# Performance work log

Hardware: AMD Instinct MI355X
Metric: run time of the kernel (lower is better)

Reference implementation:

```python
import jax, jax.numpy as jnp
import numpy as np

# --- module hyperparameters (match init_kwargs) ---
B, CIN, COUT, K = 32, 2, 2, 16
FEAT_DIM = 256
FRAME_SIZE, OVERLAP = 160, 40
NUM_FRAMES = 500
NUM_SAMPLES = NUM_FRAMES * FRAME_SIZE
FFT_SIZE = 512  # 2**ceil(log2(2*frame_size + overlap))
SHAPE_GAIN_DB = -6.0
GAIN_LIMITS_DB = (-6.0, 6.0)
LN10_DIV_20 = 0.11512925464970229


def setup_inputs() -> dict:
    key = jax.random.key(0)
    ks = jax.random.split(key, 6)
    x = jax.random.normal(ks[0], (B, CIN, NUM_SAMPLES), dtype=jnp.float32)
    features = jax.random.normal(ks[1], (B, NUM_FRAMES, FEAT_DIM), dtype=jnp.float32)
    # nn.Linear(feature_dim, in*out*K) and nn.Linear(feature_dim, out) params
    conv_kernel_w = jax.random.normal(ks[2], (COUT * CIN * K, FEAT_DIM), jnp.float32) / np.float32(np.sqrt(FEAT_DIM))
    conv_kernel_b = jax.random.normal(ks[3], (COUT * CIN * K,), jnp.float32) * 0.01
    filter_gain_w = jax.random.normal(ks[4], (COUT, FEAT_DIM), jnp.float32) / np.float32(np.sqrt(FEAT_DIM))
    filter_gain_b = jax.random.normal(ks[5], (COUT,), jnp.float32) * 0.01
    # fixed raised-cosine fade-out window (requires_grad=False buffer)
    n = jnp.arange(OVERLAP, dtype=jnp.float32)
    overlap_win = 0.5 + 0.5 * jnp.cos((n + 0.5) * jnp.pi / OVERLAP)
    return {"x": x, "features": features,
            "conv_kernel_w": conv_kernel_w, "conv_kernel_b": conv_kernel_b,
            "filter_gain_w": filter_gain_w, "filter_gain_b": filter_gain_b,
            "overlap_win": overlap_win}


def _forward(x, features, ck_w, ck_b, fg_w, fg_b, overlap_win):
    B_, F_, _ = features.shape
    log_min = GAIN_LIMITS_DB[0] * LN10_DIV_20
    log_max = GAIN_LIMITS_DB[1] * LN10_DIV_20
    gain_a = (log_max - log_min) / 2.0
    gain_b = (log_max + log_min) / 2.0
    shape_gain = min(1.0, 10.0 ** (SHAPE_GAIN_DB / 20.0))
    id_tap = K - 1 - K // 2  # padding[1]

    # per-frame kernels: (B, F, Cout, Cin, K)
    ck = (features @ ck_w.T + ck_b).reshape(B_, F_, COUT, CIN, K)
    # norm_p = 2 over (Cin, K)
    ck = ck / (1e-6 + jnp.sqrt(jnp.sum(ck * ck, axis=(-2, -1), keepdims=True)))
    idk = jnp.zeros_like(ck).at[..., id_tap].set(1.0)
    ck = shape_gain * ck + (1.0 - shape_gain) * idk
    gains = jnp.exp(gain_a * jnp.tanh(features @ fg_w.T + fg_b) + gain_b)  # (B,F,Cout)
    w = jnp.transpose(ck * gains[..., None, None], (0, 2, 3, 1, 4))  # (B,Cout,Cin,F,K)

    win1 = jnp.flip(overlap_win)  # fade-in (expansion_power == 1)
    win2 = overlap_win            # fade-out (== 1 - win1)

    # frame the input with K-1 lookback and OVERLAP lookahead samples
    xp = jnp.pad(x, ((0, 0), (0, 0), (K - 1, OVERLAP)))
    L = FRAME_SIZE + K - 1 + OVERLAP
    idx = jnp.arange(F_)[:, None] * FRAME_SIZE + jnp.arange(L)[None, :]
    frames = xp[:, :, idx]  # (B, Cin, F, L)

    # FFT convolution, summing over input channels in the frequency domain
    X = jnp.fft.rfft(frames, n=FFT_SIZE)          # (B,Cin,F,nf)
    Wf = jnp.fft.rfft(w, n=FFT_SIZE)              # (B,Cout,Cin,F,nf)
    Yf = jnp.einsum('bifn,boifn->bofn', X, Wf)
    Y = jnp.fft.irfft(Yf, n=FFT_SIZE)[..., K - 1: K - 1 + FRAME_SIZE + OVERLAP]  # (B,Cout,F,fs+ov)

    # windowed overlap-add crossfade between consecutive frame filters
    head = Y[..., :FRAME_SIZE].at[..., :OVERLAP].multiply(win1)
    tail = Y[..., FRAME_SIZE:] * win2  # (B,Cout,F,ov)
    out = head.at[:, :, 1:, :OVERLAP].add(tail[:, :, :-1])
    return out.reshape(B_, COUT, F_ * FRAME_SIZE)


def reference(x, features, conv_kernel_w, conv_kernel_b, filter_gain_w, filter_gain_b, overlap_win):
    return _forward(x, features, conv_kernel_w, conv_kernel_b, filter_gain_w, filter_gain_b, overlap_win)
```

## Files before the change

### kernel.cpp

```cpp
#include <hip/hip_runtime.h>

#define BB    32
#define NF    500
#define FRAME 160
#define OV    40
#define KK    16
#define NS    (NF * FRAME)
#define FEAT  256

#define NBODY (BB * 2 * NF * 15)
#define NOV   (BB * 2 * NF * 5)

__device__ const float GAIN_A     = 0.6907755278982137f;
__device__ const float SHAPE_GAIN = 0.5011872336272722f;

__global__ __launch_bounds__(1024) void wcalc3_kernel(
    const float* __restrict__ feats,
    const float* __restrict__ ckw,
    const float* __restrict__ ckb,
    const float* __restrict__ fgw,
    const float* __restrict__ fgb,
    float* __restrict__ wout)
{
    int tile = blockIdx.x;
    int b    = blockIdx.y;
    int f0   = tile * 64;
    int tid  = threadIdx.x;
    int w    = tid >> 6;
    int l    = tid & 63;

    __shared__ float sf[128 * 64];
    __shared__ float sr[16][64];

    int rbase = __builtin_amdgcn_readfirstlane(w * 4);
    int cout  = rbase >> 5;
    const float* gwrow = fgw + cout * FEAT;

    float acc[4] = {0.f, 0.f, 0.f, 0.f};
    float g = 0.f;

    for (int h = 0; h < 2; ++h) {
        __syncthreads();
        #pragma unroll
        for (int p = 0; p < 2; ++p) {
            int F  = p * 1024 + tid;
            int fr = F >> 5;
            int c4 = F & 31;
            int f  = f0 + fr;
            float4 v = make_float4(0.f, 0.f, 0.f, 0.f);
            if (f < NF)
                v = *(const float4*)(feats + ((size_t)(b * NF + f)) * FEAT
                                     + h * 128 + c4 * 4);
            int sw = fr ^ (c4 & 31);
            sf[(4 * c4 + 0) * 64 + sw] = v.x;
            sf[(4 * c4 + 1) * 64 + sw] = v.y;
            sf[(4 * c4 + 2) * 64 + sw] = v.z;
            sf[(4 * c4 + 3) * 64 + sw] = v.w;
        }
        __syncthreads();

        #pragma unroll 2
        for (int cl = 0; cl < 16; ++cl) {
            int k8  = cl * 8;
            int kg  = h * 128 + k8;
            int slo = (2 * cl) & 31;
            int shi = (2 * cl + 1) & 31;
            float fr8[8];
            #pragma unroll
            for (int i = 0; i < 4; ++i) fr8[i]     = sf[(k8 + i) * 64 + (l ^ slo)];
            #pragma unroll
            for (int i = 0; i < 4; ++i) fr8[4 + i] = sf[(k8 + 4 + i) * 64 + (l ^ shi)];
            #pragma unroll
            for (int r = 0; r < 4; ++r) {
                const float* wr = ckw + (size_t)(rbase + r) * FEAT + kg;
                #pragma unroll
                for (int i = 0; i < 8; ++i) acc[r] = fmaf(fr8[i], wr[i], acc[r]);
            }
            #pragma unroll
            for (int i = 0; i < 8; ++i) g = fmaf(fr8[i], gwrow[kg + i], g);
        }
    }

    #pragma unroll
    for (int r = 0; r < 4; ++r) acc[r] += ckb[rbase + r];
    g += fgb[cout];

    float ssq = 0.f;
    #pragma unroll
    for (int r = 0; r < 4; ++r) ssq = fmaf(acc[r], acc[r], ssq);
    sr[w][l] = ssq;
    __syncthreads();
    float tot = 0.f;
    #pragma unroll
    for (int j = 0; j < 8; ++j) tot += sr[cout * 8 + j][l];
    float norm = 1e-6f + sqrtf(tot);

    float gain = expf(GAIN_A * tanhf(g));
    float sc   = gain * SHAPE_GAIN / norm;
    float idv  = gain * (1.0f - SHAPE_GAIN);

    int f = f0 + l;
    if (f < NF) {
        float o[4];
        #pragma unroll
        for (int r = 0; r < 4; ++r)
            o[r] = acc[r] * sc + ((((rbase + r) & 15) == 7) ? idv : 0.f);
        float4 v;
        v.x = o[0]; v.y = o[1]; v.z = o[2]; v.w = o[3];
        *(float4*)(wout + ((size_t)(b * NF + f)) * 64 + rbase) = v;
    }
}

__global__ __launch_bounds__(256) void conv_kernel(
    const float* __restrict__ x,
    const float* __restrict__ w,
    const float* __restrict__ owin,
    float* __restrict__ out)
{
    int flat = blockIdx.x * 256 + threadIdx.x;
    if (flat < NBODY) {
        int g    = flat % 15;
        int rest = flat / 15;
        int f    = rest % NF;
        int bc   = rest / NF;
        int b = bc >> 1, cout = bc & 1;
        int s0 = f * FRAME + OV + g * 8;

        const float* xb = x + (size_t)b * 2 * NS;
        float xr[2][24];
        #pragma unroll
        for (int ci = 0; ci < 2; ++ci) {
            const float* xc = xb + (size_t)ci * NS + s0 - 16;
            #pragma unroll
            for (int c = 0; c < 6; ++c) {
                float4 v = *(const float4*)(xc + c * 4);
                xr[ci][c * 4 + 0] = v.x; xr[ci][c * 4 + 1] = v.y;
                xr[ci][c * 4 + 2] = v.z; xr[ci][c * 4 + 3] = v.w;
            }
        }
        const float4* wf = (const float4*)(w + ((size_t)(b * NF + f) * 64 + cout * 32));
        float wr[32];
        #pragma unroll
        for (int q = 0; q < 8; ++q) {
            float4 v = wf[q];
            wr[q * 4 + 0] = v.x; wr[q * 4 + 1] = v.y;
            wr[q * 4 + 2] = v.z; wr[q * 4 + 3] = v.w;
        }
        float acc[8];
        #pragma unroll
        for (int j = 0; j < 8; ++j) acc[j] = 0.f;
        #pragma unroll
        for (int ci = 0; ci < 2; ++ci)
            #pragma unroll
            for (int k = 0; k < KK; ++k) {
                float wk = wr[ci * 16 + k];
                #pragma unroll
                for (int j = 0; j < 8; ++j)
                    acc[j] = fmaf(wk, xr[ci][16 + j - k], acc[j]);
            }
        float* dst = out + (size_t)bc * NS + s0;
        float4 v0, v1;
        v0.x = acc[0]; v0.y = acc[1]; v0.z = acc[2]; v0.w = acc[3];
        v1.x = acc[4]; v1.y = acc[5]; v1.z = acc[6]; v1.w = acc[7];
        *(float4*)(dst)     = v0;
        *(float4*)(dst + 4) = v1;
    } else {
        int flat2 = flat - NBODY;
        int g    = flat2 % 5;
        int rest = flat2 / 5;
        int f    = rest % NF;
        int bc   = rest / NF;
        int b = bc >> 1, cout = bc & 1;
        int t0 = g * 8;
        int s0 = f * FRAME + t0;

        const float* xb = x + (size_t)b * 2 * NS;
        float xr[2][24];
        #pragma unroll
        for (int ci = 0; ci < 2; ++ci) {
            const float* xc = xb + (size_t)ci * NS + s0 - 16;
            #pragma unroll
            for (int c = 0; c < 6; ++c) {
                if (s0 - 16 + c * 4 >= 0) {
                    float4 v = *(const float4*)(xc + c * 4);
                    xr[ci][c * 4 + 0] = v.x; xr[ci][c * 4 + 1] = v.y;
                    xr[ci][c * 4 + 2] = v.z; xr[ci][c * 4 + 3] = v.w;
                } else {
                    xr[ci][c * 4 + 0] = 0.f; xr[ci][c * 4 + 1] = 0.f;
                    xr[ci][c * 4 + 2] = 0.f; xr[ci][c * 4 + 3] = 0.f;
                }
            }
        }

        const float* wfb = w + ((size_t)(b * NF + f) * 64 + cout * 32);
        float res[8];
        #pragma unroll
        for (int j = 0; j < 8; ++j) res[j] = 0.f;

        float wr[32];
        if (f > 0) {
            const float4* wp = (const float4*)(wfb - 64);
            #pragma unroll
            for (int q = 0; q < 8; ++q) {
                float4 v = wp[q];
                wr[q * 4 + 0] = v.x; wr[q * 4 + 1] = v.y;
                wr[q * 4 + 2] = v.z; wr[q * 4 + 3] = v.w;
            }
            float acc[8];
            #pragma unroll
            for (int j = 0; j < 8; ++j) acc[j] = 0.f;
            #pragma unroll
            for (int ci = 0; ci < 2; ++ci)
                #pragma unroll
                for (int k = 0; k < KK; ++k) {
                    float wk = wr[ci * 16 + k];
                    #pragma unroll
                    for (int j = 0; j < 8; ++j)
                        acc[j] = fmaf(wk, xr[ci][16 + j - k], acc[j]);
                }
            #pragma unroll
            for (int j = 0; j < 8; ++j) res[j] = owin[t0 + j] * acc[j];
        }
        {
            const float4* wf = (const float4*)wfb;
            #pragma unroll
            for (int q = 0; q < 8; ++q) {
                float4 v = wf[q];
                wr[q * 4 + 0] = v.x; wr[q * 4 + 1] = v.y;
                wr[q * 4 + 2] = v.z; wr[q * 4 + 3] = v.w;
            }
            float acc[8];
            #pragma unroll
            for (int j = 0; j < 8; ++j) acc[j] = 0.f;
            #pragma unroll
            for (int ci = 0; ci < 2; ++ci)
                #pragma unroll
                for (int k = 0; k < KK; ++k) {
                    float wk = wr[ci * 16 + k];
                    #pragma unroll
                    for (int j = 0; j < 8; ++j)
                        acc[j] = fmaf(wk, xr[ci][16 + j - k], acc[j]);
                }
            #pragma unroll
            for (int j = 0; j < 8; ++j)
                res[j] = fmaf(owin[(OV - 1) - (t0 + j)], acc[j], res[j]);
        }
        float* dst = out + (size_t)bc * NS + s0;
        float4 v0, v1;
        v0.x = res[0]; v0.y = res[1]; v0.z = res[2]; v0.w = res[3];
        v1.x = res[4]; v1.y = res[5]; v1.z = res[6]; v1.w = res[7];
        *(float4*)(dst)     = v0;
        *(float4*)(dst + 4) = v1;
    }
}

extern "C" void kernel_launch(void* const* d_in, const int* in_sizes, int n_in,
                              void* d_out, int out_size, void* d_ws, size_t ws_size,
                              hipStream_t stream) {
    const float* x     = (const float*)d_in[0];
    const float* feats = (const float*)d_in[1];
    const float* ckw   = (const float*)d_in[2];
    const float* ckb   = (const float*)d_in[3];
    const float* fgw   = (const float*)d_in[4];
    const float* fgb   = (const float*)d_in[5];
    const float* owin  = (const float*)d_in[6];
    float* out  = (float*)d_out;
    float* wbuf = (float*)d_ws;

    hipLaunchKernelGGL(wcalc3_kernel, dim3(8, BB), dim3(1024), 0, stream,
                       feats, ckw, ckb, fgw, fgb, wbuf);

    hipLaunchKernelGGL(conv_kernel, dim3((NBODY + NOV) / 256), dim3(256), 0, stream,
                       x, wbuf, owin, out);
}
```

Baseline: 123.5 us.

## Split weight kernel across output channels and reuse input loads for both outputs

The weight-generation kernel is now launched with a third grid dimension, one per output channel, using 512-thread blocks instead of 1024. This doubles the number of blocks and halves the per-block norm reduction. The conv kernel has each thread compute both output channels from a single load of the input samples, halving the redundant x reads, and loads the crossfade window as vectors. The cost is more registers per conv thread and half as many threads, which may reduce occupancy.

```diff
diff --git a/kernel.cpp b/kernel.cpp
--- a/kernel.cpp
+++ b/kernel.cpp
@@ -8,13 +8,13 @@
 #define NS    (NF * FRAME)
 #define FEAT  256
 
-#define NBODY (BB * 2 * NF * 15)
-#define NOV   (BB * 2 * NF * 5)
+#define NBODY2 (BB * NF * 15)
+#define NOV2   (BB * NF * 5)
 
 __device__ const float GAIN_A     = 0.6907755278982137f;
 __device__ const float SHAPE_GAIN = 0.5011872336272722f;
 
-__global__ __launch_bounds__(1024) void wcalc3_kernel(
+__global__ __launch_bounds__(512) void wcalc4_kernel(
     const float* __restrict__ feats,
     const float* __restrict__ ckw,
     const float* __restrict__ ckb,
@@ -24,17 +24,17 @@
 {
     int tile = blockIdx.x;
     int b    = blockIdx.y;
+    int z    = blockIdx.z;
     int f0   = tile * 64;
     int tid  = threadIdx.x;
     int w    = tid >> 6;
     int l    = tid & 63;
 
     __shared__ float sf[128 * 64];
-    __shared__ float sr[16][64];
-
-    int rbase = __builtin_amdgcn_readfirstlane(w * 4);
-    int cout  = rbase >> 5;
-    const float* gwrow = fgw + cout * FEAT;
+    __shared__ float sr[8][64];
+
+    int rbase = __builtin_amdgcn_readfirstlane(z * 32 + w * 4);
+    const float* gwrow = fgw + z * FEAT;
 
     float acc[4] = {0.f, 0.f, 0.f, 0.f};
     float g = 0.f;
@@ -42,8 +42,8 @@
     for (int h = 0; h < 2; ++h) {
         __syncthreads();
         #pragma unroll
-        for (int p = 0; p < 2; ++p) {
-            int F  = p * 1024 + tid;
+        for (int p = 0; p < 4; ++p) {
+            int F  = p * 512 + tid;
             int fr = F >> 5;
             int c4 = F & 31;
             int f  = f0 + fr;
@@ -51,7 +51,7 @@
             if (f < NF)
                 v = *(const float4*)(feats + ((size_t)(b * NF + f)) * FEAT
                                      + h * 128 + c4 * 4);
-            int sw = fr ^ (c4 & 31);
+            int sw = fr ^ c4;
             sf[(4 * c4 + 0) * 64 + sw] = v.x;
             sf[(4 * c4 + 1) * 64 + sw] = v.y;
             sf[(4 * c4 + 2) * 64 + sw] = v.z;
@@ -83,7 +83,7 @@
 
     #pragma unroll
     for (int r = 0; r < 4; ++r) acc[r] += ckb[rbase + r];
-    g += fgb[cout];
+    g += fgb[z];
 
     float ssq = 0.f;
     #pragma unroll
@@ -92,7 +92,7 @@
     __syncthreads();
     float tot = 0.f;
     #pragma unroll
-    for (int j = 0; j < 8; ++j) tot += sr[cout * 8 + j][l];
+    for (int j = 0; j < 8; ++j) tot += sr[j][l];
     float norm = 1e-6f + sqrtf(tot);
 
     float gain = expf(GAIN_A * tanhf(g));
@@ -111,20 +111,19 @@
     }
 }
 
-__global__ __launch_bounds__(256) void conv_kernel(
+__global__ __launch_bounds__(256) void conv2_kernel(
     const float* __restrict__ x,
     const float* __restrict__ w,
     const float* __restrict__ owin,
     float* __restrict__ out)
 {
     int flat = blockIdx.x * 256 + threadIdx.x;
-    if (flat < NBODY) {
+    if (flat < NBODY2) {
         int g    = flat % 15;
         int rest = flat / 15;
         int f    = rest % NF;
-        int bc   = rest / NF;
-        int b = bc >> 1, cout = bc & 1;
-        int s0 = f * FRAME + OV + g * 8;
+        int b    = rest / NF;
+        int s0   = f * FRAME + OV + g * 8;
 
         const float* xb = x + (size_t)b * 2 * NS;
         float xr[2][24];
@@ -138,41 +137,44 @@
                 xr[ci][c * 4 + 2] = v.z; xr[ci][c * 4 + 3] = v.w;
             }
         }
-        const float4* wf = (const float4*)(w + ((size_t)(b * NF + f) * 64 + cout * 32));
-        float wr[32];
-        #pragma unroll
-        for (int q = 0; q < 8; ++q) {
-            float4 v = wf[q];
-            wr[q * 4 + 0] = v.x; wr[q * 4 + 1] = v.y;
-            wr[q * 4 + 2] = v.z; wr[q * 4 + 3] = v.w;
-        }
-        float acc[8];
-        #pragma unroll
-        for (int j = 0; j < 8; ++j) acc[j] = 0.f;
-        #pragma unroll
-        for (int ci = 0; ci < 2; ++ci)
-            #pragma unroll
-            for (int k = 0; k < KK; ++k) {
-                float wk = wr[ci * 16 + k];
-                #pragma unroll
-                for (int j = 0; j < 8; ++j)
-                    acc[j] = fmaf(wk, xr[ci][16 + j - k], acc[j]);
-            }
-        float* dst = out + (size_t)bc * NS + s0;
-        float4 v0, v1;
-        v0.x = acc[0]; v0.y = acc[1]; v0.z = acc[2]; v0.w = acc[3];
-        v1.x = acc[4]; v1.y = acc[5]; v1.z = acc[6]; v1.w = acc[7];
-        *(float4*)(dst)     = v0;
-        *(float4*)(dst + 4) = v1;
+        const float* wfb = w + (size_t)(b * NF + f) * 64;
+        #pragma unroll
+        for (int cout = 0; cout < 2; ++cout) {
+            const float4* wf = (const float4*)(wfb + cout * 32);
+            float wr[32];
+            #pragma unroll
+            for (int q = 0; q < 8; ++q) {
+                float4 v = wf[q];
+                wr[q * 4 + 0] = v.x; wr[q * 4 + 1] = v.y;
+                wr[q * 4 + 2] = v.z; wr[q * 4 + 3] = v.w;
+            }
+            float acc[8];
+            #pragma unroll
+            for (int j = 0; j < 8; ++j) acc[j] = 0.f;
+            #pragma unroll
+            for (int ci = 0; ci < 2; ++ci)
+                #pragma unroll
+                for (int k = 0; k < KK; ++k) {
+                    float wk = wr[ci * 16 + k];
+                    #pragma unroll
+                    for (int j = 0; j < 8; ++j)
+                        acc[j] = fmaf(wk, xr[ci][16 + j - k], acc[j]);
+                }
+            float* dst = out + (size_t)(b * 2 + cout) * NS + s0;
+            float4 v0, v1;
+            v0.x = acc[0]; v0.y = acc[1]; v0.z = acc[2]; v0.w = acc[3];
+            v1.x = acc[4]; v1.y = acc[5]; v1.z = acc[6]; v1.w = acc[7];
+            *(float4*)(dst)     = v0;
+            *(float4*)(dst + 4) = v1;
+        }
     } else {
-        int flat2 = flat - NBODY;
+        int flat2 = flat - NBODY2;
         int g    = flat2 % 5;
         int rest = flat2 / 5;
         int f    = rest % NF;
-        int bc   = rest / NF;
-        int b = bc >> 1, cout = bc & 1;
-        int t0 = g * 8;
-        int s0 = f * FRAME + t0;
+        int b    = rest / NF;
+        int t0   = g * 8;
+        int s0   = f * FRAME + t0;
 
         const float* xb = x + (size_t)b * 2 * NS;
         float xr[2][24];
@@ -192,65 +194,80 @@
             }
         }
 
-        const float* wfb = w + ((size_t)(b * NF + f) * 64 + cout * 32);
-        float res[8];
-        #pragma unroll
-        for (int j = 0; j < 8; ++j) res[j] = 0.f;
-
-        float wr[32];
-        if (f > 0) {
-            const float4* wp = (const float4*)(wfb - 64);
-            #pragma unroll
-            for (int q = 0; q < 8; ++q) {
-                float4 v = wp[q];
-                wr[q * 4 + 0] = v.x; wr[q * 4 + 1] = v.y;
-                wr[q * 4 + 2] = v.z; wr[q * 4 + 3] = v.w;
-            }
-            float acc[8];
-            #pragma unroll
-            for (int j = 0; j < 8; ++j) acc[j] = 0.f;
-            #pragma unroll
-            for (int ci = 0; ci < 2; ++ci)
-                #pragma unroll
-                for (int k = 0; k < KK; ++k) {
-                    float wk = wr[ci * 16 + k];
+        float o_tail[8], o_head[8];
+        {
+            float4 a = *(const float4*)(owin + t0);
+            float4 c = *(const float4*)(owin + t0 + 4);
+            o_tail[0] = a.x; o_tail[1] = a.y; o_tail[2] = a.z; o_tail[3] = a.w;
+            o_tail[4] = c.x; o_tail[5] = c.y; o_tail[6] = c.z; o_tail[7] = c.w;
+            float4 d = *(const float4*)(owin + (32 - t0));
+            float4 e = *(const float4*)(owin + (36 - t0));
+            o_head[0] = e.w; o_head[1] = e.z; o_head[2] = e.y; o_head[3] = e.x;
+            o_head[4] = d.w; o_head[5] = d.z; o_head[6] = d.y; o_head[7] = d.x;
+        }
+
+        const float* wfb = w + (size_t)(b * NF + f) * 64;
+        #pragma unroll
+        for (int cout = 0; cout < 2; ++cout) {
+            float res[8];
+            #pragma unroll
+            for (int j = 0; j < 8; ++j) res[j] = 0.f;
+
+            float wr[32];
+            if (f > 0) {
+                const float4* wp = (const float4*)(wfb - 64 + cout * 32);
+                #pragma unroll
+                for (int q = 0; q < 8; ++q) {
+                    float4 v = wp[q];
+                    wr[q * 4 + 0] = v.x; wr[q * 4 + 1] = v.y;
+                    wr[q * 4 + 2] = v.z; wr[q * 4 + 3] = v.w;
+                }
+                float acc[8];
+                #pragma unroll
+                for (int j = 0; j < 8; ++j) acc[j] = 0.f;
+                #pragma unroll
+                for (int ci = 0; ci < 2; ++ci)
                     #pragma unroll
-                    for (int j = 0; j < 8; ++j)
-                        acc[j] = fmaf(wk, xr[ci][16 + j - k], acc[j]);
-                }
-            #pragma unroll
-            for (int j = 0; j < 8; ++j) res[j] = owin[t0 + j] * acc[j];
-        }
-        {
-            const float4* wf = (const float4*)wfb;
-            #pragma unroll
-            for (int q = 0; q < 8; ++q) {
-                float4 v = wf[q];
-                wr[q * 4 + 0] = v.x; wr[q * 4 + 1] = v.y;
-                wr[q * 4 + 2] = v.z; wr[q * 4 + 3] = v.w;
-            }
-            float acc[8];
-            #pragma unroll
-            for (int j = 0; j < 8; ++j) acc[j] = 0.f;
-            #pragma unroll
-            for (int ci = 0; ci < 2; ++ci)
-                #pragma unroll
-                for (int k = 0; k < KK; ++k) {
-                    float wk = wr[ci * 16 + k];
+                    for (int k = 0; k < KK; ++k) {
+                        float wk = wr[ci * 16 + k];
+                        #pragma unroll
+                        for (int j = 0; j < 8; ++j)
+                            acc[j] = fmaf(wk, xr[ci][16 + j - k], acc[j]);
+                    }
+                #pragma unroll
+                for (int j = 0; j < 8; ++j) res[j] = o_tail[j] * acc[j];
+            }
+            {
+                const float4* wf = (const float4*)(wfb + cout * 32);
+                #pragma unroll
+                for (int q = 0; q < 8; ++q) {
+                    float4 v = wf[q];
+                    wr[q * 4 + 0] = v.x; wr[q * 4 + 1] = v.y;
+                    wr[q * 4 + 2] = v.z; wr[q * 4 + 3] = v.w;
+                }
+                float acc[8];
+                #pragma unroll
+                for (int j = 0; j < 8; ++j) acc[j] = 0.f;
+                #pragma unroll
+                for (int ci = 0; ci < 2; ++ci)
                     #pragma unroll
-                    for (int j = 0; j < 8; ++j)
-                        acc[j] = fmaf(wk, xr[ci][16 + j - k], acc[j]);
-                }
-            #pragma unroll
-            for (int j = 0; j < 8; ++j)
-                res[j] = fmaf(owin[(OV - 1) - (t0 + j)], acc[j], res[j]);
-        }
-        float* dst = out + (size_t)bc * NS + s0;
-        float4 v0, v1;
-        v0.x = res[0]; v0.y = res[1]; v0.z = res[2]; v0.w = res[3];
-        v1.x = res[4]; v1.y = res[5]; v1.z = res[6]; v1.w = res[7];
-        *(float4*)(dst)     = v0;
-        *(float4*)(dst + 4) = v1;
+                    for (int k = 0; k < KK; ++k) {
+                        float wk = wr[ci * 16 + k];
+                        #pragma unroll
+                        for (int j = 0; j < 8; ++j)
+                            acc[j] = fmaf(wk, xr[ci][16 + j - k], acc[j]);
+                    }
+                #pragma unroll
+                for (int j = 0; j < 8; ++j)
+                    res[j] = fmaf(o_head[j], acc[j], res[j]);
+            }
+            float* dst = out + (size_t)(b * 2 + cout) * NS + s0;
+            float4 v0, v1;
+            v0.x = res[0]; v0.y = res[1]; v0.z = res[2]; v0.w = res[3];
+            v1.x = res[4]; v1.y = res[5]; v1.z = res[6]; v1.w = res[7];
+            *(float4*)(dst)     = v0;
+            *(float4*)(dst + 4) = v1;
+        }
     }
 }
 
@@ -267,9 +284,9 @@
     float* out  = (float*)d_out;
     float* wbuf = (float*)d_ws;
 
-    hipLaunchKernelGGL(wcalc3_kernel, dim3(8, BB), dim3(1024), 0, stream,
+    hipLaunchKernelGGL(wcalc4_kernel, dim3(8, BB, 2), dim3(512), 0, stream,
                        feats, ckw, ckb, fgw, fgb, wbuf);
 
-    hipLaunchKernelGGL(conv_kernel, dim3((NBODY + NOV) / 256), dim3(256), 0, stream,
+    hipLaunchKernelGGL(conv2_kernel, dim3((NBODY2 + NOV2) / 256), dim3(256), 0, stream,
                        x, wbuf, owin, out);
 }
```

New measurement: 119.2 us. 1.04x faster.
